# Kernel optimization log

Measured on AMD Instinct MI355X. Metric: run time of the kernel, lower is better.

## Reference

```python
import jax, jax.numpy as jnp
import numpy as np

N_NODES = 50000
N_EDGES = 1600000
IN_FEATS = 128
HIDDEN = 16
HEADS = 8
SLOPE = 0.2


def setup_inputs() -> dict:
    key = jax.random.key(0)
    ks = jax.random.split(key, 9)
    feat = jax.random.normal(ks[0], (N_NODES, IN_FEATS), dtype=jnp.float32)
    edge_src = jax.random.randint(ks[1], (N_EDGES,), 0, N_NODES, dtype=jnp.int32)
    edge_dst = jax.random.randint(ks[2], (N_EDGES,), 0, N_NODES, dtype=jnp.int32)
    # layer 0: in=128 -> H*F=128 ; layer 1: in=128 (concat of layer 0) -> 128
    s0 = 1.0 / np.sqrt(IN_FEATS)
    W0 = jax.random.normal(ks[3], (IN_FEATS, HEADS * HIDDEN), dtype=jnp.float32) * s0
    al0 = jax.random.normal(ks[4], (HEADS, HIDDEN), dtype=jnp.float32) * 0.1
    ar0 = jax.random.normal(ks[5], (HEADS, HIDDEN), dtype=jnp.float32) * 0.1
    W1 = jax.random.normal(ks[6], (HEADS * HIDDEN, HEADS * HIDDEN), dtype=jnp.float32) * s0
    al1 = jax.random.normal(ks[7], (HEADS, HIDDEN), dtype=jnp.float32) * 0.1
    ar1 = jax.random.normal(ks[8], (HEADS, HIDDEN), dtype=jnp.float32) * 0.1
    return {"feat": feat, "edge_src": edge_src, "edge_dst": edge_dst,
            "W0": W0, "al0": al0, "ar0": ar0, "W1": W1, "al1": al1, "ar1": ar1}


def _gat_conv(feat, W, al, ar, src, dst):
    """One DGL-style GATConv: no bias, no residual, no dropout, no activation."""
    n = feat.shape[0]
    h = (feat @ W).reshape(n, HEADS, HIDDEN)              # [N,H,F]
    el = jnp.sum(h * al, axis=-1)                          # [N,H]
    er = jnp.sum(h * ar, axis=-1)                          # [N,H]
    e = jax.nn.leaky_relu(el[src] + er[dst], negative_slope=SLOPE)  # [E,H]
    # edge softmax over incoming edges of each dst node
    m = jax.ops.segment_max(e, dst, num_segments=n)        # [N,H]
    ex = jnp.exp(e - m[dst])                               # [E,H]
    denom = jax.ops.segment_sum(ex, dst, num_segments=n)   # [N,H]
    alpha = ex / jnp.where(denom[dst] > 0, denom[dst], 1.0)
    # message passing: gather src features, weight, scatter-add to dst
    out = jax.ops.segment_sum(h[src] * alpha[:, :, None], dst, num_segments=n)
    return out                                             # [N,H,F]


def reference(feat, edge_src, edge_dst, W0, al0, ar0, W1, al1, ar1):
    n = feat.shape[0]
    # step 1 + concat (flatten heads)
    x = _gat_conv(feat, W0, al0, ar0, edge_src, edge_dst).reshape(n, HEADS * HIDDEN)
    # step 2 + concat
    x = _gat_conv(x, W1, al1, ar1, edge_src, edge_dst).reshape(n, HEADS * HIDDEN)
    return x
```

## Files before the change

kernel.cpp:

```cpp
#include <hip/hip_runtime.h>
#include <hip/hip_bf16.h>


#define HEADS 8
#define HID 16
#define HF 128
#define SLOPE 0.2f

#define BSHIFT 8
#define BRANGE 256
#define CHUNK 4096

typedef __attribute__((ext_vector_type(8))) short bf16x8;
typedef __attribute__((ext_vector_type(4))) float f32x4;

static __device__ __forceinline__ unsigned int f2bf(float f) {
    unsigned int u = __float_as_uint(f);
    u += 0x7fffu + ((u >> 16) & 1u);
    return u >> 16;
}


__global__ __launch_bounds__(512) void bhist_kernel(
    const int* __restrict__ dst, int* __restrict__ bhistT, int E, int nb, int nblk) {
    __shared__ int h[BRANGE];
    int t = threadIdx.x;
    if (t < BRANGE) h[t] = 0;
    __syncthreads();
    int base = blockIdx.x * CHUNK;
    int end = base + CHUNK; if (end > E) end = E;
    for (int i = base + t; i < end; i += 512)
        atomicAdd(&h[dst[i] >> BSHIFT], 1);
    __syncthreads();
    if (t < nb) bhistT[(size_t)t * nblk + blockIdx.x] = h[t];
}

__global__ __launch_bounds__(64) void bscan1_kernel(
    const int* __restrict__ bhistT, int* __restrict__ boffT,
    int* __restrict__ btot, int nblk) {
    int b = blockIdx.x;
    int l = threadIdx.x;
    int carry = 0;
    for (int c0 = 0; c0 < nblk; c0 += 64) {
        int blk = c0 + l;
        int v = (blk < nblk) ? bhistT[(size_t)b * nblk + blk] : 0;
        int x = v;
        #pragma unroll
        for (int off = 1; off < 64; off <<= 1) {
            int y = __shfl_up(x, off, 64);
            if (l >= off) x += y;
        }
        if (blk < nblk) boffT[(size_t)b * nblk + blk] = carry + x - v;
        carry += __shfl(x, 63);
    }
    if (l == 0) btot[b] = carry;
}

__global__ __launch_bounds__(256) void bscan2_kernel(
    const int* __restrict__ btot, int* __restrict__ bbase,
    int* __restrict__ rowptr, int nb, int N, int E) {
    __shared__ int s[256];
    int t = threadIdx.x;
    s[t] = (t < nb) ? btot[t] : 0;
    __syncthreads();
    #pragma unroll
    for (int off = 1; off < 256; off <<= 1) {
        int v = (t >= off) ? s[t - off] : 0;
        __syncthreads();
        s[t] += v;
        __syncthreads();
    }
    int excl = (t == 0) ? 0 : s[t - 1];
    if (t < nb) bbase[t] = excl;
    if (t == 0) { bbase[nb] = E; rowptr[N] = E; }
}

__global__ __launch_bounds__(512) void bucket_scatter_kernel(
    const int* __restrict__ src, const int* __restrict__ dst,
    const int* __restrict__ bhistT, const int* __restrict__ boffT,
    const int* __restrict__ bbase, int* __restrict__ stage,
    int E, int nb, int nblk) {
    __shared__ int lscan[BRANGE];
    __shared__ int lcur[BRANGE];
    __shared__ int gbase[BRANGE];
    __shared__ int sstage[CHUNK];
    int t = threadIdx.x;
    int blk = blockIdx.x;
    int base = blk * CHUNK;
    int end = base + CHUNK; if (end > E) end = E;

    if (t < 256) lscan[t] = (t < nb) ? bhistT[(size_t)t * nblk + blk] : 0;
    __syncthreads();
    #pragma unroll
    for (int off = 1; off < 256; off <<= 1) {
        int v = 0;
        if (t < 256 && t >= off) v = lscan[t - off];
        __syncthreads();
        if (t < 256) lscan[t] += v;
        __syncthreads();
    }
    int ex = 0;
    if (t < 256) ex = (t == 0) ? 0 : lscan[t - 1];
    __syncthreads();
    if (t < 256) {
        lcur[t] = ex;
        lscan[t] = ex;
        if (t < nb) gbase[t] = bbase[t] + boffT[(size_t)t * nblk + blk];
    }
    __syncthreads();

    for (int i = base + t; i < end; i += 512) {
        int d = dst[i];
        int b = d >> BSHIFT;
        int pos = atomicAdd(&lcur[b], 1);
        sstage[pos] = (src[i] & 0xFFFF) | ((d & (BRANGE - 1)) << 16) | (b << 24);
    }
    __syncthreads();

    int total = end - base;
    for (int i = t; i < total; i += 512) {
        int p = sstage[i];
        int b = ((unsigned)p) >> 24;
        int gpos = gbase[b] + (i - lscan[b]);
        stage[gpos] = p;
    }
}

__global__ __launch_bounds__(512) void bucket_csr_kernel(
    const int* __restrict__ stage, const int* __restrict__ bbase,
    int* __restrict__ rowptr, unsigned short* __restrict__ col, int N, int nb) {
    __shared__ int hist[BRANGE];
    __shared__ int lscan[BRANGE];
    __shared__ int lcur[BRANGE];
    int b = blockIdx.x;
    int t = threadIdx.x;
    int e0 = bbase[b], e1 = bbase[b + 1];
    if (t < BRANGE) hist[t] = 0;
    __syncthreads();
    for (int i = e0 + t; i < e1; i += 512)
        atomicAdd(&hist[(stage[i] >> 16) & (BRANGE - 1)], 1);
    __syncthreads();
    if (t < 256) lscan[t] = hist[t];
    __syncthreads();
    #pragma unroll
    for (int off = 1; off < 256; off <<= 1) {
        int v = 0;
        if (t < 256 && t >= off) v = lscan[t - off];
        __syncthreads();
        if (t < 256) lscan[t] += v;
        __syncthreads();
    }
    if (t < 256) {
        int ex = (t == 0) ? 0 : lscan[t - 1];
        lcur[t] = ex;
        int node = (b << BSHIFT) + t;
        if (node < N) rowptr[node] = e0 + ex;
    }
    __syncthreads();
    for (int i = e0 + t; i < e1; i += 512) {
        int p = stage[i];
        int pos = e0 + atomicAdd(&lcur[(p >> 16) & (BRANGE - 1)], 1);
        col[pos] = (unsigned short)(p & 0xFFFF);
    }
}


__global__ __launch_bounds__(256) void wtrans_kernel(const float* __restrict__ W,
                                                     unsigned short* __restrict__ Wtb) {
    int gid = blockIdx.x * 256 + threadIdx.x;
    int c = gid >> 3;
    int k0 = (gid & 7) * 16;
    #pragma unroll
    for (int q = 0; q < 4; ++q) {
        int k = k0 + q * 4;
        ushort4 o = make_ushort4(
            (unsigned short)f2bf(W[(k + 0) * HF + c]),
            (unsigned short)f2bf(W[(k + 1) * HF + c]),
            (unsigned short)f2bf(W[(k + 2) * HF + c]),
            (unsigned short)f2bf(W[(k + 3) * HF + c]));
        *(ushort4*)(Wtb + (size_t)c * HF + k) = o;
    }
}


template <bool XBF16>
__global__ __launch_bounds__(256) void gemm_mfma_kernel(
    const void* __restrict__ Xv, const unsigned short* __restrict__ Wtb,
    const float* __restrict__ AL, const float* __restrict__ AR,
    unsigned short* __restrict__ Hb, float* __restrict__ EL,
    float* __restrict__ ER, int n) {
    __shared__ __align__(16) unsigned short xs[64 * HF];
    __shared__ __align__(16) unsigned short ws[HF * HF];
    int t = threadIdx.x;
    int row0 = blockIdx.x * 64;

    {
        int r = t >> 2;
        int gr = row0 + r;
        unsigned int rowbase = r * 256;
        unsigned int sw = (r & 7) << 4;
        if (XBF16) {
            unsigned int kb0 = (t & 3) * 64;
            const char* src = (const char*)Xv + (size_t)gr * 256 + kb0;
            #pragma unroll
            for (int i = 0; i < 4; ++i) {
                int4 v = (gr < n) ? *(const int4*)(src + i * 16)
                                  : make_int4(0, 0, 0, 0);
                *(int4*)((char*)xs + rowbase + ((kb0 + i * 16) ^ sw)) = v;
            }
        } else {
            int k0 = (t & 3) * 32;
            float4 f[8];
            if (gr < n) {
                const float4* p = (const float4*)((const float*)Xv + (size_t)gr * HF + k0);
                #pragma unroll
                for (int i = 0; i < 8; ++i) f[i] = p[i];
            } else {
                #pragma unroll
                for (int i = 0; i < 8; ++i) f[i] = make_float4(0.f, 0.f, 0.f, 0.f);
            }
            #pragma unroll
            for (int g2 = 0; g2 < 4; ++g2) {
                float4 a = f[g2 * 2], b = f[g2 * 2 + 1];
                int4 pk;
                pk.x = (int)(f2bf(a.x) | (f2bf(a.y) << 16));
                pk.y = (int)(f2bf(a.z) | (f2bf(a.w) << 16));
                pk.z = (int)(f2bf(b.x) | (f2bf(b.y) << 16));
                pk.w = (int)(f2bf(b.z) | (f2bf(b.w) << 16));
                unsigned int addr = rowbase + ((unsigned)((k0 + g2 * 8) * 2) ^ sw);
                *(int4*)((char*)xs + addr) = pk;
            }
        }
    }
    {
        int c = t >> 1;
        unsigned int kb0 = (t & 1) * 128;
        const int4* src = (const int4*)((const char*)Wtb + (size_t)c * 256 + kb0);
        unsigned int sw = (c & 7) << 4;
        #pragma unroll
        for (int i = 0; i < 8; ++i) {
            int4 v = src[i];
            unsigned int addr = c * 256 + ((kb0 + i * 16) ^ sw);
            *(int4*)((char*)ws + addr) = v;
        }
    }
    __syncthreads();

    int wv = t >> 6;
    int l = t & 63;
    int lr = l & 15;
    int g = l >> 4;

    bf16x8 bfr[4];
    {
        int r = wv * 16 + lr;
        unsigned int rowbase = r * 256;
        unsigned int sw = (r & 7) << 4;
        #pragma unroll
        for (int s = 0; s < 4; ++s) {
            unsigned int kbyte = (unsigned)((s * 32 + g * 8) * 2);
            bfr[s] = *(bf16x8*)((char*)xs + rowbase + (kbyte ^ sw));
        }
    }

    f32x4 acc[8];
    #pragma unroll
    for (int ct = 0; ct < 8; ++ct) acc[ct] = (f32x4){0.f, 0.f, 0.f, 0.f};

    #pragma unroll
    for (int ct = 0; ct < 8; ++ct) {
        int c = ct * 16 + lr;
        unsigned int rowbase = c * 256;
        unsigned int sw = (c & 7) << 4;
        #pragma unroll
        for (int s = 0; s < 4; ++s) {
            unsigned int kbyte = (unsigned)((s * 32 + g * 8) * 2);
            bf16x8 af = *(bf16x8*)((char*)ws + rowbase + (kbyte ^ sw));
            acc[ct] = __builtin_amdgcn_mfma_f32_16x16x32_bf16(af, bfr[s], acc[ct], 0, 0, 0);
        }
    }

    int grow = row0 + wv * 16 + lr;
    bool valid = grow < n;

    if (valid) {
        #pragma unroll
        for (int ct = 0; ct < 8; ++ct) {
            ushort4 hb4 = make_ushort4(
                (unsigned short)f2bf(acc[ct][0]), (unsigned short)f2bf(acc[ct][1]),
                (unsigned short)f2bf(acc[ct][2]), (unsigned short)f2bf(acc[ct][3]));
            *(ushort4*)(Hb + (size_t)grow * HF + ct * 16 + g * 4) = hb4;
        }
    }

    #pragma unroll
    for (int ct = 0; ct < 8; ++ct) {
        float e1 = 0.f, e2 = 0.f;
        #pragma unroll
        for (int rg = 0; rg < 4; ++rg) {
            float alv = AL[ct * 16 + g * 4 + rg];
            float arv = AR[ct * 16 + g * 4 + rg];
            e1 += acc[ct][rg] * alv;
            e2 += acc[ct][rg] * arv;
        }
        e1 += __shfl_xor(e1, 16); e1 += __shfl_xor(e1, 32);
        e2 += __shfl_xor(e2, 16); e2 += __shfl_xor(e2, 32);
        if (g == 0 && valid) {
            EL[grow * HEADS + ct] = e1;
            ER[grow * HEADS + ct] = e2;
        }
    }
}


template <bool OBF16>
__global__ __launch_bounds__(256) void gat_aggregate_kernel(
    const unsigned int* __restrict__ HbU,
    const float* __restrict__ EL, const float* __restrict__ ER,
    const int* __restrict__ rowptr, const unsigned short* __restrict__ col,
    void* __restrict__ OUT, int n) {
    int wid = (int)((blockIdx.x * blockDim.x + threadIdx.x) >> 6);
    if (wid >= n) return;
    int lane = threadIdx.x & 63;
    int s0 = rowptr[wid], s1 = rowptr[wid + 1];
    if (s1 == s0) {
        if (OBF16) ((unsigned int*)OUT)[(size_t)wid * 64 + lane] = 0u;
        else ((float2*)OUT)[(size_t)wid * 64 + lane] = make_float2(0.f, 0.f);
        return;
    }

    int h = lane & 7;
    int j = lane >> 3;
    int hC = lane >> 3;
    float er_h = ER[wid * HEADS + h];

    float accx = 0.f, accy = 0.f;
    float dpart = 0.f;

    for (int base = s0; base < s1; base += 8) {
        int i = base + j;
        int icl = i < s1 ? i : s1 - 1;
        int sj = (int)col[icl];
        float e = EL[sj * HEADS + h] + er_h;
        e = fmaxf(e, SLOPE * e);
        float w = __expf(e);
        if (i >= s1) w = 0.f;
        dpart += w;

        if (base + 8 <= s1) {
            #pragma unroll
            for (int jj = 0; jj < 8; ++jj) {
                float wC = __shfl(w, jj * 8 + hC);
                int s = __builtin_amdgcn_readlane(sj, jj * 8);
                unsigned int pv = HbU[(size_t)s * 64 + lane];
                accx += wC * __uint_as_float(pv << 16);
                accy += wC * __uint_as_float(pv & 0xffff0000u);
            }
        } else {
            int ne = s1 - base;
            for (int jj = 0; jj < ne; ++jj) {
                float wC = __shfl(w, jj * 8 + hC);
                int s = __builtin_amdgcn_readlane(sj, jj * 8);
                unsigned int pv = HbU[(size_t)s * 64 + lane];
                accx += wC * __uint_as_float(pv << 16);
                accy += wC * __uint_as_float(pv & 0xffff0000u);
            }
        }
    }

    dpart += __shfl_xor(dpart, 8);
    dpart += __shfl_xor(dpart, 16);
    dpart += __shfl_xor(dpart, 32);
    float rC = 1.f / __shfl(dpart, hC);

    if (OBF16) {
        unsigned int o = f2bf(accx * rC) | (f2bf(accy * rC) << 16);
        ((unsigned int*)OUT)[(size_t)wid * 64 + lane] = o;
    } else {
        ((float2*)OUT)[(size_t)wid * 64 + lane] = make_float2(accx * rC, accy * rC);
    }
}


extern "C" void kernel_launch(void* const* d_in, const int* in_sizes, int n_in,
                              void* d_out, int out_size, void* d_ws, size_t ws_size,
                              hipStream_t stream) {
    const float* feat = (const float*)d_in[0];
    const int*   esrc = (const int*)d_in[1];
    const int*   edst = (const int*)d_in[2];
    const float* W0   = (const float*)d_in[3];
    const float* al0  = (const float*)d_in[4];
    const float* ar0  = (const float*)d_in[5];
    const float* W1   = (const float*)d_in[6];
    const float* al1  = (const float*)d_in[7];
    const float* ar1  = (const float*)d_in[8];
    float* out = (float*)d_out;

    const int N = in_sizes[0] / HF;
    const int E = in_sizes[1];
    const int nb = (N + BRANGE - 1) >> BSHIFT;
    const int nblk = (E + CHUNK - 1) / CHUNK;

    char* w = (char*)d_ws;
    auto alloc = [&](size_t bytes) -> void* {
        void* p = (void*)w;
        w += (bytes + 255) & ~(size_t)255;
        return p;
    };
    unsigned short* hb   = (unsigned short*)alloc((size_t)N * HF * 2);
    unsigned short* x1b  = (unsigned short*)alloc((size_t)N * HF * 2);
    float* el_buf = (float*)alloc((size_t)N * HEADS * 4);
    float* er_buf = (float*)alloc((size_t)N * HEADS * 4);
    int*   rowptr = (int*)alloc((size_t)(N + 1) * 4);
    unsigned short* col = (unsigned short*)alloc((size_t)E * 2);
    int*   bhistT = (int*)alloc((size_t)nb * nblk * 4);
    int*   boffT  = (int*)alloc((size_t)nb * nblk * 4);
    int*   btot   = (int*)alloc((size_t)nb * 4);
    int*   bbase  = (int*)alloc((size_t)(nb + 1) * 4);
    unsigned short* wtb0 = (unsigned short*)alloc((size_t)HF * HF * 2);
    unsigned short* wtb1 = (unsigned short*)alloc((size_t)HF * HF * 2);
    int*   stage  = (int*)alloc((size_t)E * 4);

    wtrans_kernel<<<4, 256, 0, stream>>>(W0, wtb0);
    wtrans_kernel<<<4, 256, 0, stream>>>(W1, wtb1);

    bhist_kernel<<<nblk, 512, 0, stream>>>(edst, bhistT, E, nb, nblk);
    bscan1_kernel<<<nb, 64, 0, stream>>>(bhistT, boffT, btot, nblk);
    bscan2_kernel<<<1, 256, 0, stream>>>(btot, bbase, rowptr, nb, N, E);
    bucket_scatter_kernel<<<nblk, 512, 0, stream>>>(esrc, edst, bhistT, boffT,
                                                    bbase, stage, E, nb, nblk);
    bucket_csr_kernel<<<nb, 512, 0, stream>>>(stage, bbase, rowptr, col, N, nb);

    int gGemm = (N + 63) / 64;
    int gAgg  = (N * 64 + 255) / 256;

    gemm_mfma_kernel<false><<<gGemm, 256, 0, stream>>>(feat, wtb0, al0, ar0,
                                                       hb, el_buf, er_buf, N);
    gat_aggregate_kernel<true><<<gAgg, 256, 0, stream>>>(
        (const unsigned int*)hb, el_buf, er_buf, rowptr, col, x1b, N);

    gemm_mfma_kernel<true><<<gGemm, 256, 0, stream>>>(x1b, wtb1, al1, ar1,
                                                      hb, el_buf, er_buf, N);
    gat_aggregate_kernel<false><<<gAgg, 256, 0, stream>>>(
        (const unsigned int*)hb, el_buf, er_buf, rowptr, col, out, N);
}
```

Before: 222.6 us.

## Fuse layer-0 GEMM, edge bucket histogram and W1 transpose into one launch

```diff
diff --git a/kernel.cpp b/kernel.cpp
--- a/kernel.cpp
+++ b/kernel.cpp
@@ -21,178 +21,15 @@
 }
 
 
-__global__ __launch_bounds__(512) void bhist_kernel(
-    const int* __restrict__ dst, int* __restrict__ bhistT, int E, int nb, int nblk) {
-    __shared__ int h[BRANGE];
-    int t = threadIdx.x;
-    if (t < BRANGE) h[t] = 0;
-    __syncthreads();
-    int base = blockIdx.x * CHUNK;
-    int end = base + CHUNK; if (end > E) end = E;
-    for (int i = base + t; i < end; i += 512)
-        atomicAdd(&h[dst[i] >> BSHIFT], 1);
-    __syncthreads();
-    if (t < nb) bhistT[(size_t)t * nblk + blockIdx.x] = h[t];
-}
-
-__global__ __launch_bounds__(64) void bscan1_kernel(
-    const int* __restrict__ bhistT, int* __restrict__ boffT,
-    int* __restrict__ btot, int nblk) {
-    int b = blockIdx.x;
-    int l = threadIdx.x;
-    int carry = 0;
-    for (int c0 = 0; c0 < nblk; c0 += 64) {
-        int blk = c0 + l;
-        int v = (blk < nblk) ? bhistT[(size_t)b * nblk + blk] : 0;
-        int x = v;
-        #pragma unroll
-        for (int off = 1; off < 64; off <<= 1) {
-            int y = __shfl_up(x, off, 64);
-            if (l >= off) x += y;
-        }
-        if (blk < nblk) boffT[(size_t)b * nblk + blk] = carry + x - v;
-        carry += __shfl(x, 63);
-    }
-    if (l == 0) btot[b] = carry;
-}
-
-__global__ __launch_bounds__(256) void bscan2_kernel(
-    const int* __restrict__ btot, int* __restrict__ bbase,
-    int* __restrict__ rowptr, int nb, int N, int E) {
-    __shared__ int s[256];
-    int t = threadIdx.x;
-    s[t] = (t < nb) ? btot[t] : 0;
-    __syncthreads();
-    #pragma unroll
-    for (int off = 1; off < 256; off <<= 1) {
-        int v = (t >= off) ? s[t - off] : 0;
-        __syncthreads();
-        s[t] += v;
-        __syncthreads();
-    }
-    int excl = (t == 0) ? 0 : s[t - 1];
-    if (t < nb) bbase[t] = excl;
-    if (t == 0) { bbase[nb] = E; rowptr[N] = E; }
-}
-
-__global__ __launch_bounds__(512) void bucket_scatter_kernel(
-    const int* __restrict__ src, const int* __restrict__ dst,
-    const int* __restrict__ bhistT, const int* __restrict__ boffT,
-    const int* __restrict__ bbase, int* __restrict__ stage,
-    int E, int nb, int nblk) {
-    __shared__ int lscan[BRANGE];
-    __shared__ int lcur[BRANGE];
-    __shared__ int gbase[BRANGE];
-    __shared__ int sstage[CHUNK];
-    int t = threadIdx.x;
-    int blk = blockIdx.x;
-    int base = blk * CHUNK;
-    int end = base + CHUNK; if (end > E) end = E;
-
-    if (t < 256) lscan[t] = (t < nb) ? bhistT[(size_t)t * nblk + blk] : 0;
-    __syncthreads();
-    #pragma unroll
-    for (int off = 1; off < 256; off <<= 1) {
-        int v = 0;
-        if (t < 256 && t >= off) v = lscan[t - off];
-        __syncthreads();
-        if (t < 256) lscan[t] += v;
-        __syncthreads();
-    }
-    int ex = 0;
-    if (t < 256) ex = (t == 0) ? 0 : lscan[t - 1];
-    __syncthreads();
-    if (t < 256) {
-        lcur[t] = ex;
-        lscan[t] = ex;
-        if (t < nb) gbase[t] = bbase[t] + boffT[(size_t)t * nblk + blk];
-    }
-    __syncthreads();
-
-    for (int i = base + t; i < end; i += 512) {
-        int d = dst[i];
-        int b = d >> BSHIFT;
-        int pos = atomicAdd(&lcur[b], 1);
-        sstage[pos] = (src[i] & 0xFFFF) | ((d & (BRANGE - 1)) << 16) | (b << 24);
-    }
-    __syncthreads();
-
-    int total = end - base;
-    for (int i = t; i < total; i += 512) {
-        int p = sstage[i];
-        int b = ((unsigned)p) >> 24;
-        int gpos = gbase[b] + (i - lscan[b]);
-        stage[gpos] = p;
-    }
-}
-
-__global__ __launch_bounds__(512) void bucket_csr_kernel(
-    const int* __restrict__ stage, const int* __restrict__ bbase,
-    int* __restrict__ rowptr, unsigned short* __restrict__ col, int N, int nb) {
-    __shared__ int hist[BRANGE];
-    __shared__ int lscan[BRANGE];
-    __shared__ int lcur[BRANGE];
-    int b = blockIdx.x;
-    int t = threadIdx.x;
-    int e0 = bbase[b], e1 = bbase[b + 1];
-    if (t < BRANGE) hist[t] = 0;
-    __syncthreads();
-    for (int i = e0 + t; i < e1; i += 512)
-        atomicAdd(&hist[(stage[i] >> 16) & (BRANGE - 1)], 1);
-    __syncthreads();
-    if (t < 256) lscan[t] = hist[t];
-    __syncthreads();
-    #pragma unroll
-    for (int off = 1; off < 256; off <<= 1) {
-        int v = 0;
-        if (t < 256 && t >= off) v = lscan[t - off];
-        __syncthreads();
-        if (t < 256) lscan[t] += v;
-        __syncthreads();
-    }
-    if (t < 256) {
-        int ex = (t == 0) ? 0 : lscan[t - 1];
-        lcur[t] = ex;
-        int node = (b << BSHIFT) + t;
-        if (node < N) rowptr[node] = e0 + ex;
-    }
-    __syncthreads();
-    for (int i = e0 + t; i < e1; i += 512) {
-        int p = stage[i];
-        int pos = e0 + atomicAdd(&lcur[(p >> 16) & (BRANGE - 1)], 1);
-        col[pos] = (unsigned short)(p & 0xFFFF);
-    }
-}
-
-
-__global__ __launch_bounds__(256) void wtrans_kernel(const float* __restrict__ W,
-                                                     unsigned short* __restrict__ Wtb) {
-    int gid = blockIdx.x * 256 + threadIdx.x;
-    int c = gid >> 3;
-    int k0 = (gid & 7) * 16;
-    #pragma unroll
-    for (int q = 0; q < 4; ++q) {
-        int k = k0 + q * 4;
-        ushort4 o = make_ushort4(
-            (unsigned short)f2bf(W[(k + 0) * HF + c]),
-            (unsigned short)f2bf(W[(k + 1) * HF + c]),
-            (unsigned short)f2bf(W[(k + 2) * HF + c]),
-            (unsigned short)f2bf(W[(k + 3) * HF + c]));
-        *(ushort4*)(Wtb + (size_t)c * HF + k) = o;
-    }
-}
-
-
 template <bool XBF16>
-__global__ __launch_bounds__(256) void gemm_mfma_kernel(
+static __device__ __forceinline__ void gemm_body(
+    int blk, unsigned short* xs, unsigned short* ws,
     const void* __restrict__ Xv, const unsigned short* __restrict__ Wtb,
     const float* __restrict__ AL, const float* __restrict__ AR,
     unsigned short* __restrict__ Hb, float* __restrict__ EL,
     float* __restrict__ ER, int n) {
-    __shared__ __align__(16) unsigned short xs[64 * HF];
-    __shared__ __align__(16) unsigned short ws[HF * HF];
     int t = threadIdx.x;
-    int row0 = blockIdx.x * 64;
+    int row0 = blk * 64;
 
     {
         int r = t >> 2;
@@ -313,6 +150,200 @@
 }
 
 
+static __device__ __forceinline__ void wtrans_body(
+    int blk, const float* __restrict__ W, unsigned short* __restrict__ Wtb) {
+    int gid = blk * 256 + threadIdx.x;
+    int c = gid >> 3;
+    int k0 = (gid & 7) * 16;
+    #pragma unroll
+    for (int q = 0; q < 4; ++q) {
+        int k = k0 + q * 4;
+        ushort4 o = make_ushort4(
+            (unsigned short)f2bf(W[(k + 0) * HF + c]),
+            (unsigned short)f2bf(W[(k + 1) * HF + c]),
+            (unsigned short)f2bf(W[(k + 2) * HF + c]),
+            (unsigned short)f2bf(W[(k + 3) * HF + c]));
+        *(ushort4*)(Wtb + (size_t)c * HF + k) = o;
+    }
+}
+
+
+__global__ __launch_bounds__(256) void fused0_kernel(
+    const float* __restrict__ X, const unsigned short* __restrict__ Wtb0,
+    const float* __restrict__ AL, const float* __restrict__ AR,
+    unsigned short* __restrict__ Hb, float* __restrict__ EL,
+    float* __restrict__ ER, int n, int gGemm,
+    const int* __restrict__ edst, int* __restrict__ bhistT, int E, int nb, int nblk,
+    const float* __restrict__ W1, unsigned short* __restrict__ wtb1) {
+    __shared__ __align__(16) unsigned char lds[48 * 1024];
+    int b = blockIdx.x;
+    if (b < gGemm) {
+        gemm_body<false>(b, (unsigned short*)lds, (unsigned short*)(lds + 16384),
+                         X, Wtb0, AL, AR, Hb, EL, ER, n);
+    } else if (b < gGemm + nblk) {
+        int blk = b - gGemm;
+        int* h = (int*)lds;
+        int t = threadIdx.x;
+        h[t] = 0;
+        __syncthreads();
+        int base = blk * CHUNK;
+        int end = base + CHUNK; if (end > E) end = E;
+        for (int i = base + t; i < end; i += 256)
+            atomicAdd(&h[edst[i] >> BSHIFT], 1);
+        __syncthreads();
+        if (t < nb) bhistT[(size_t)t * nblk + blk] = h[t];
+    } else {
+        wtrans_body(b - gGemm - nblk, W1, wtb1);
+    }
+}
+
+
+__global__ __launch_bounds__(256) void wtrans_kernel(const float* __restrict__ W,
+                                                     unsigned short* __restrict__ Wtb) {
+    wtrans_body(blockIdx.x, W, Wtb);
+}
+
+template <bool XBF16>
+__global__ __launch_bounds__(256) void gemm_mfma_kernel(
+    const void* __restrict__ Xv, const unsigned short* __restrict__ Wtb,
+    const float* __restrict__ AL, const float* __restrict__ AR,
+    unsigned short* __restrict__ Hb, float* __restrict__ EL,
+    float* __restrict__ ER, int n) {
+    __shared__ __align__(16) unsigned short xs[64 * HF];
+    __shared__ __align__(16) unsigned short ws[HF * HF];
+    gemm_body<XBF16>(blockIdx.x, xs, ws, Xv, Wtb, AL, AR, Hb, EL, ER, n);
+}
+
+__global__ __launch_bounds__(64) void bscan1_kernel(
+    const int* __restrict__ bhistT, int* __restrict__ boffT,
+    int* __restrict__ btot, int nblk) {
+    int b = blockIdx.x;
+    int l = threadIdx.x;
+    int carry = 0;
+    for (int c0 = 0; c0 < nblk; c0 += 64) {
+        int blk = c0 + l;
+        int v = (blk < nblk) ? bhistT[(size_t)b * nblk + blk] : 0;
+        int x = v;
+        #pragma unroll
+        for (int off = 1; off < 64; off <<= 1) {
+            int y = __shfl_up(x, off, 64);
+            if (l >= off) x += y;
+        }
+        if (blk < nblk) boffT[(size_t)b * nblk + blk] = carry + x - v;
+        carry += __shfl(x, 63);
+    }
+    if (l == 0) btot[b] = carry;
+}
+
+__global__ __launch_bounds__(256) void bscan2_kernel(
+    const int* __restrict__ btot, int* __restrict__ bbase,
+    int* __restrict__ rowptr, int nb, int N, int E) {
+    __shared__ int s[256];
+    int t = threadIdx.x;
+    s[t] = (t < nb) ? btot[t] : 0;
+    __syncthreads();
+    #pragma unroll
+    for (int off = 1; off < 256; off <<= 1) {
+        int v = (t >= off) ? s[t - off] : 0;
+        __syncthreads();
+        s[t] += v;
+        __syncthreads();
+    }
+    int excl = (t == 0) ? 0 : s[t - 1];
+    if (t < nb) bbase[t] = excl;
+    if (t == 0) { bbase[nb] = E; rowptr[N] = E; }
+}
+
+__global__ __launch_bounds__(512) void bucket_scatter_kernel(
+    const int* __restrict__ src, const int* __restrict__ dst,
+    const int* __restrict__ bhistT, const int* __restrict__ boffT,
+    const int* __restrict__ bbase, int* __restrict__ stage,
+    int E, int nb, int nblk) {
+    __shared__ int lscan[BRANGE];
+    __shared__ int lcur[BRANGE];
+    __shared__ int gbase[BRANGE];
+    __shared__ int sstage[CHUNK];
+    int t = threadIdx.x;
+    int blk = blockIdx.x;
+    int base = blk * CHUNK;
+    int end = base + CHUNK; if (end > E) end = E;
+
+    if (t < 256) lscan[t] = (t < nb) ? bhistT[(size_t)t * nblk + blk] : 0;
+    __syncthreads();
+    #pragma unroll
+    for (int off = 1; off < 256; off <<= 1) {
+        int v = 0;
+        if (t < 256 && t >= off) v = lscan[t - off];
+        __syncthreads();
+        if (t < 256) lscan[t] += v;
+        __syncthreads();
+    }
+    int ex = 0;
+    if (t < 256) ex = (t == 0) ? 0 : lscan[t - 1];
+    __syncthreads();
+    if (t < 256) {
+        lcur[t] = ex;
+        lscan[t] = ex;
+        if (t < nb) gbase[t] = bbase[t] + boffT[(size_t)t * nblk + blk];
+    }
+    __syncthreads();
+
+    for (int i = base + t; i < end; i += 512) {
+        int d = dst[i];
+        int b = d >> BSHIFT;
+        int pos = atomicAdd(&lcur[b], 1);
+        sstage[pos] = (src[i] & 0xFFFF) | ((d & (BRANGE - 1)) << 16) | (b << 24);
+    }
+    __syncthreads();
+
+    int total = end - base;
+    for (int i = t; i < total; i += 512) {
+        int p = sstage[i];
+        int b = ((unsigned)p) >> 24;
+        int gpos = gbase[b] + (i - lscan[b]);
+        stage[gpos] = p;
+    }
+}
+
+__global__ __launch_bounds__(512) void bucket_csr_kernel(
+    const int* __restrict__ stage, const int* __restrict__ bbase,
+    int* __restrict__ rowptr, unsigned short* __restrict__ col, int N, int nb) {
+    __shared__ int hist[BRANGE];
+    __shared__ int lscan[BRANGE];
+    __shared__ int lcur[BRANGE];
+    int b = blockIdx.x;
+    int t = threadIdx.x;
+    int e0 = bbase[b], e1 = bbase[b + 1];
+    if (t < BRANGE) hist[t] = 0;
+    __syncthreads();
+    for (int i = e0 + t; i < e1; i += 512)
+        atomicAdd(&hist[(stage[i] >> 16) & (BRANGE - 1)], 1);
+    __syncthreads();
+    if (t < 256) lscan[t] = hist[t];
+    __syncthreads();
+    #pragma unroll
+    for (int off = 1; off < 256; off <<= 1) {
+        int v = 0;
+        if (t < 256 && t >= off) v = lscan[t - off];
+        __syncthreads();
+        if (t < 256) lscan[t] += v;
+        __syncthreads();
+    }
+    if (t < 256) {
+        int ex = (t == 0) ? 0 : lscan[t - 1];
+        lcur[t] = ex;
+        int node = (b << BSHIFT) + t;
+        if (node < N) rowptr[node] = e0 + ex;
+    }
+    __syncthreads();
+    for (int i = e0 + t; i < e1; i += 512) {
+        int p = stage[i];
+        int pos = e0 + atomicAdd(&lcur[(p >> 16) & (BRANGE - 1)], 1);
+        col[pos] = (unsigned short)(p & 0xFFFF);
+    }
+}
+
+
 template <bool OBF16>
 __global__ __launch_bounds__(256) void gat_aggregate_kernel(
     const unsigned int* __restrict__ HbU,
@@ -421,21 +452,21 @@
     unsigned short* wtb1 = (unsigned short*)alloc((size_t)HF * HF * 2);
     int*   stage  = (int*)alloc((size_t)E * 4);
 
+    int gGemm = (N + 63) / 64;
+    int gAgg  = (N * 64 + 255) / 256;
+
     wtrans_kernel<<<4, 256, 0, stream>>>(W0, wtb0);
-    wtrans_kernel<<<4, 256, 0, stream>>>(W1, wtb1);
-
-    bhist_kernel<<<nblk, 512, 0, stream>>>(edst, bhistT, E, nb, nblk);
+
+    fused0_kernel<<<gGemm + nblk + 4, 256, 0, stream>>>(
+        feat, wtb0, al0, ar0, hb, el_buf, er_buf, N, gGemm,
+        edst, bhistT, E, nb, nblk, W1, wtb1);
+
     bscan1_kernel<<<nb, 64, 0, stream>>>(bhistT, boffT, btot, nblk);
     bscan2_kernel<<<1, 256, 0, stream>>>(btot, bbase, rowptr, nb, N, E);
     bucket_scatter_kernel<<<nblk, 512, 0, stream>>>(esrc, edst, bhistT, boffT,
                                                     bbase, stage, E, nb, nblk);
     bucket_csr_kernel<<<nb, 512, 0, stream>>>(stage, bbase, rowptr, col, N, nb);
 
-    int gGemm = (N + 63) / 64;
-    int gAgg  = (N * 64 + 255) / 256;
-
-    gemm_mfma_kernel<false><<<gGemm, 256, 0, stream>>>(feat, wtb0, al0, ar0,
-                                                       hb, el_buf, er_buf, N);
     gat_aggregate_kernel<true><<<gAgg, 256, 0, stream>>>(
         (const unsigned int*)hb, el_buf, er_buf, rowptr, col, x1b, N);
 
```

New measurement: 215.3 us. 3.3% less time.
